# Performance work log

Hardware: AMD Instinct MI355X
Metric: run time of the kernel (lower is better)

## Reference

```python
import jax, jax.numpy as jnp
import numpy as np

NEG_INF = -9e15  # matches -9000000000000000.0 in the torch source


def setup_inputs() -> dict:
    key = jax.random.key(0)
    k1, k2, k3, k4 = jax.random.split(key, 4)
    B, H, N, D = 4, 8, 2048, 64
    queries = jax.random.normal(k1, (B, H, N, D), dtype=jnp.float32)
    keys = jax.random.normal(k2, (B, H, N, D), dtype=jnp.float32)
    values = jax.random.normal(k3, (B, H, N, D), dtype=jnp.float32)
    adj = jax.random.randint(k4, (N, N), 0, 2, dtype=jnp.int32)
    return {"queries": queries, "keys": keys, "values": values, "adj": adj}


def reference(queries, keys, values, adj):
    B, H, N, D = queries.shape
    # e = Q K^T / 8  (hard-coded divisor == sqrt(64))
    e = jnp.einsum("bhnd,bhmd->bhnm", queries, keys) / 8.0
    # graph-adjacency mask (adj [N,N] broadcasts over batch and heads)
    att = jnp.where(adj > 0, e, NEG_INF)
    att = jax.nn.softmax(att, axis=-1)
    # dropout p=0.0 / eval mode -> identity
    h_prime = jnp.einsum("bhnm,bhmd->bhnd", att, values)  # [B,H,N,D]
    # original uses .view (flat reshape), NOT a permute
    return h_prime.reshape(N, B, H, D)
```

## Files before the change

kernel.cpp:

```cpp
#include <hip/hip_runtime.h>
#include <math.h>

typedef short short8 __attribute__((ext_vector_type(8)));
typedef float float4_t __attribute__((ext_vector_type(4)));
typedef unsigned uint2_t __attribute__((ext_vector_type(2)));
typedef unsigned short ushort_t;

#define BH   32
#define N_   2048
#define D_   64
#define NCH  32
#define LDP  72
#define KV_ELEMS (BH * N_ * D_)
#define OFF_VF  (KV_ELEMS * 2)
#define OFF_MSK (KV_ELEMS * 4)
#define QSCALE 0.18033688f

__device__ __forceinline__ unsigned pack_bf16(float a, float b) {
  union { float f; unsigned u; } ua{a}, ub{b};
  return __builtin_amdgcn_perm(ub.u + 0x8000u, ua.u + 0x8000u, 0x07060302u);
}

__global__ __launch_bounds__(256) void prep_kernel(
    const float* __restrict__ K, const float* __restrict__ V,
    const int* __restrict__ adj, ushort_t* __restrict__ Kf,
    ushort_t* __restrict__ Vf, unsigned long long* __restrict__ msk) {
  __shared__ __align__(16) float Tc[64 * 68];
  const int blk = blockIdx.x, t = threadIdx.x;

  if (blk < 2048) {
    const bool isK = blk < 1024;
    const int b = isK ? blk : blk - 1024;
    const float* src = (isK ? K : V) + (b >> 5) * (N_ * D_) + (b & 31) * 64 * D_;
#pragma unroll
    for (int i = 0; i < 4; ++i) {
      int idx = i * 256 + t;
      int row = idx >> 4, c4 = (idx & 15) * 4;
      *(float4_t*)&Tc[row * 68 + c4] = *(const float4_t*)(src + row * D_ + c4);
    }
    __syncthreads();
    ushort_t* dst = (isK ? Kf : Vf) + b * 4096;
#pragma unroll
    for (int e = 0; e < 2; ++e) {
      int u = t * 2 + e;
      int g = u >> 6, lane = u & 63;
      int ks = g >> 2, quad = lane >> 4, l16 = lane & 15;
      float v[8];
      if (isK) {
        int nt = g & 3;
        const float* rp = &Tc[(nt * 16 + l16) * 68 + ks * 32 + quad * 8];
        float4_t a = *(const float4_t*)(rp);
        float4_t bq = *(const float4_t*)(rp + 4);
#pragma unroll
        for (int j = 0; j < 4; ++j) { v[j] = a[j]; v[4 + j] = bq[j]; }
      } else {
        int dt = g & 3, d = dt * 16 + l16;
#pragma unroll
        for (int j = 0; j < 8; ++j) {
          int key = 16 * (j & 3) + ks * 8 + quad * 2 + (j >> 2);
          v[j] = Tc[key * 68 + d];
        }
      }
      union { short8 s; unsigned u4[4]; } h;
      h.u4[0] = pack_bf16(v[0], v[1]); h.u4[1] = pack_bf16(v[2], v[3]);
      h.u4[2] = pack_bf16(v[4], v[5]); h.u4[3] = pack_bf16(v[6], v[7]);
      *(short8*)(dst + u * 8) = h.s;
    }
  } else {
    const int row = (blk - 2048) * 4 + (t >> 6);
    const int lane = t & 63;
    unsigned long long keep = 0;
#pragma unroll 8
    for (int i = 0; i < 32; ++i) {
      int a = adj[row * N_ + i * 64 + lane];
      unsigned long long b = __ballot(a > 0);
      if (lane == i) keep = b;
    }
    if (lane < 32) msk[row * 32 + lane] = keep;
  }
}

__global__ __launch_bounds__(128) void attn_main(
    const float* __restrict__ Q, const ushort_t* __restrict__ Kf,
    const ushort_t* __restrict__ Vf, const unsigned long long* __restrict__ msk,
    float* __restrict__ O) {
  __shared__ __align__(16) ushort_t kbuf[512 * 8];
  __shared__ __align__(16) ushort_t vbuf[512 * 8];
  __shared__ __align__(16) ushort_t lds_p[2][2][16 * LDP];

  const int t    = threadIdx.x;
  const int w    = t >> 6;
  const int lane = t & 63;
  const int quad = lane >> 4;
  const int l16  = lane & 15;
  const int bh   = blockIdx.x & (BH - 1);
  const int qt   = blockIdx.x >> 5;
  const int base = bh * (N_ * D_);
  const int qrow0 = qt * 64 + w * 32;

  const ushort_t* Kfb = Kf + (bh * 32) * 4096;
  const ushort_t* Vfb = Vf + (bh * 32) * 4096;

  short8 qf[2][2];
#pragma unroll
  for (int qg = 0; qg < 2; ++qg)
#pragma unroll
    for (int ks = 0; ks < 2; ++ks) {
      const float* qp = Q + base + (qrow0 + qg * 16 + l16) * D_ + ks * 32 + quad * 8;
      float4_t f0 = *(const float4_t*)(qp);
      float4_t f1 = *(const float4_t*)(qp + 4);
      union { short8 s; unsigned u[4]; } h;
      h.u[0] = pack_bf16(f0[0] * QSCALE, f0[1] * QSCALE);
      h.u[1] = pack_bf16(f0[2] * QSCALE, f0[3] * QSCALE);
      h.u[2] = pack_bf16(f1[0] * QSCALE, f1[1] * QSCALE);
      h.u[3] = pack_bf16(f1[2] * QSCALE, f1[3] * QSCALE);
      qf[qg][ks] = h.s;
    }

  float4_t oacc[2][4];
  float lsum[2][4];
#pragma unroll
  for (int qg = 0; qg < 2; ++qg) {
#pragma unroll
    for (int dt = 0; dt < 4; ++dt) oacc[qg][dt] = (float4_t){0.f, 0.f, 0.f, 0.f};
#pragma unroll
    for (int r = 0; r < 4; ++r) lsum[qg][r] = 0.f;
  }

  for (int c = 0; c < NCH; ++c) {
    __syncthreads();

    const ushort_t* kg = Kfb + c * 4096;
    const ushort_t* vg = Vfb + c * 4096;
#pragma unroll
    for (int i = 0; i < 4; ++i) {
      int u = i * 128 + t;
      *(short8*)(kbuf + u * 8) = *(const short8*)(kg + u * 8);
      *(short8*)(vbuf + u * 8) = *(const short8*)(vg + u * 8);
    }
    __syncthreads();

    short8 kf[4][2], vf[4][2];
#pragma unroll
    for (int nt = 0; nt < 4; ++nt)
#pragma unroll
      for (int ks = 0; ks < 2; ++ks) {
        kf[nt][ks] = *(const short8*)(kbuf + ((ks * 4 + nt) * 64 + lane) * 8);
        vf[nt][ks] = *(const short8*)(vbuf + ((ks * 4 + nt) * 64 + lane) * 8);
      }

    float4_t sacc[2][4];
#pragma unroll
    for (int qg = 0; qg < 2; ++qg)
#pragma unroll
      for (int nt = 0; nt < 4; ++nt) {
        float4_t acc = (float4_t){0.f, 0.f, 0.f, 0.f};
#pragma unroll
        for (int ks = 0; ks < 2; ++ks)
          acc = __builtin_amdgcn_mfma_f32_16x16x32_bf16(qf[qg][ks], kf[nt][ks], acc, 0, 0, 0);
        sacc[qg][nt] = acc;
      }

#pragma unroll
    for (int qg = 0; qg < 2; ++qg) {
      const int qrowq = qrow0 + qg * 16 + quad * 4;
#pragma unroll
      for (int r = 0; r < 4; ++r) {
        unsigned long long m = msk[(qrowq + r) * 32 + c];
        unsigned long long sh = m >> l16;
        unsigned lo = (unsigned)sh, hi = (unsigned)(sh >> 32);
        float p0 = (lo & 1u)       ? exp2f(sacc[qg][0][r]) : 0.f;
        float p1 = (lo & 0x10000u) ? exp2f(sacc[qg][1][r]) : 0.f;
        float p2 = (hi & 1u)       ? exp2f(sacc[qg][2][r]) : 0.f;
        float p3 = (hi & 0x10000u) ? exp2f(sacc[qg][3][r]) : 0.f;
        lsum[qg][r] += (p0 + p1) + (p2 + p3);
        uint2_t d2;
        d2.x = pack_bf16(p0, p1);
        d2.y = pack_bf16(p2, p3);
        *(uint2_t*)&lds_p[w][qg][(quad * 4 + r) * LDP + (l16 << 2)] = d2;
      }
    }

#pragma unroll
    for (int qg = 0; qg < 2; ++qg)
#pragma unroll
      for (int ks = 0; ks < 2; ++ks) {
        short8 pf = *(const short8*)&lds_p[w][qg][l16 * LDP + ks * 32 + quad * 8];
#pragma unroll
        for (int dt = 0; dt < 4; ++dt)
          oacc[qg][dt] = __builtin_amdgcn_mfma_f32_16x16x32_bf16(pf, vf[dt][ks], oacc[qg][dt], 0, 0, 0);
      }
  }

#pragma unroll
  for (int qg = 0; qg < 2; ++qg)
#pragma unroll
    for (int r = 0; r < 4; ++r) {
      float l = lsum[qg][r];
      l += __shfl_xor(l, 1);
      l += __shfl_xor(l, 2);
      l += __shfl_xor(l, 4);
      l += __shfl_xor(l, 8);
      float inv = 1.f / l;
      int qi = qrow0 + qg * 16 + quad * 4 + r;
#pragma unroll
      for (int dt = 0; dt < 4; ++dt)
        O[base + qi * D_ + dt * 16 + l16] = oacc[qg][dt][r] * inv;
    }
}

extern "C" void kernel_launch(void* const* d_in, const int* in_sizes, int n_in,
                              void* d_out, int out_size, void* d_ws, size_t ws_size,
                              hipStream_t stream) {
  const float* Q  = (const float*)d_in[0];
  const float* K  = (const float*)d_in[1];
  const float* V  = (const float*)d_in[2];
  const int* adj  = (const int*)d_in[3];
  float* O        = (float*)d_out;
  ushort_t* Kf    = (ushort_t*)d_ws;
  ushort_t* Vf    = (ushort_t*)((char*)d_ws + OFF_VF);
  unsigned long long* msk = (unsigned long long*)((char*)d_ws + OFF_MSK);

  prep_kernel<<<2560, 256, 0, stream>>>(K, V, adj, Kf, Vf, msk);
  attn_main<<<1024, 128, 0, stream>>>(Q, Kf, Vf, msk, O);
}
```

Before: 188.8 us.

## Load K/V fragments directly from global, drop LDS staging and block barriers

The attention kernel now uses 256 threads per block, with each wave handling 16 query rows instead of 32. K and V MFMA fragments are read straight from global memory in their pre-swizzled layout, so the shared-memory staging buffers and both __syncthreads per chunk are gone. The goal is to cut barrier stalls and LDS traffic and to raise occupancy through launch bounds (256,4) and fewer registers. The cost is that every wave now fetches the full K/V chunk from global/L2 on its own, which raises cache traffic and halves K/V reuse per wave.

```diff
diff --git a/kernel.cpp b/kernel.cpp
--- a/kernel.cpp
+++ b/kernel.cpp
@@ -80,13 +80,11 @@
   }
 }
 
-__global__ __launch_bounds__(128) void attn_main(
+__global__ __launch_bounds__(256, 4) void attn_main(
     const float* __restrict__ Q, const ushort_t* __restrict__ Kf,
     const ushort_t* __restrict__ Vf, const unsigned long long* __restrict__ msk,
     float* __restrict__ O) {
-  __shared__ __align__(16) ushort_t kbuf[512 * 8];
-  __shared__ __align__(16) ushort_t vbuf[512 * 8];
-  __shared__ __align__(16) ushort_t lds_p[2][2][16 * LDP];
+  __shared__ __align__(16) ushort_t lds_p[4][16 * LDP];
 
   const int t    = threadIdx.x;
   const int w    = t >> 6;
@@ -96,117 +94,98 @@
   const int bh   = blockIdx.x & (BH - 1);
   const int qt   = blockIdx.x >> 5;
   const int base = bh * (N_ * D_);
-  const int qrow0 = qt * 64 + w * 32;
+  const int qrow0 = qt * 64 + w * 16;
 
   const ushort_t* Kfb = Kf + (bh * 32) * 4096;
   const ushort_t* Vfb = Vf + (bh * 32) * 4096;
-
-  short8 qf[2][2];
-#pragma unroll
-  for (int qg = 0; qg < 2; ++qg)
-#pragma unroll
-    for (int ks = 0; ks < 2; ++ks) {
-      const float* qp = Q + base + (qrow0 + qg * 16 + l16) * D_ + ks * 32 + quad * 8;
-      float4_t f0 = *(const float4_t*)(qp);
-      float4_t f1 = *(const float4_t*)(qp + 4);
-      union { short8 s; unsigned u[4]; } h;
-      h.u[0] = pack_bf16(f0[0] * QSCALE, f0[1] * QSCALE);
-      h.u[1] = pack_bf16(f0[2] * QSCALE, f0[3] * QSCALE);
-      h.u[2] = pack_bf16(f1[0] * QSCALE, f1[1] * QSCALE);
-      h.u[3] = pack_bf16(f1[2] * QSCALE, f1[3] * QSCALE);
-      qf[qg][ks] = h.s;
-    }
-
-  float4_t oacc[2][4];
-  float lsum[2][4];
-#pragma unroll
-  for (int qg = 0; qg < 2; ++qg) {
-#pragma unroll
-    for (int dt = 0; dt < 4; ++dt) oacc[qg][dt] = (float4_t){0.f, 0.f, 0.f, 0.f};
-#pragma unroll
-    for (int r = 0; r < 4; ++r) lsum[qg][r] = 0.f;
-  }
+  const unsigned long long* mrow = msk + (qrow0 + quad * 4) * 32;
+
+  short8 qf[2];
+#pragma unroll
+  for (int ks = 0; ks < 2; ++ks) {
+    const float* qp = Q + base + (qrow0 + l16) * D_ + ks * 32 + quad * 8;
+    float4_t f0 = *(const float4_t*)(qp);
+    float4_t f1 = *(const float4_t*)(qp + 4);
+    union { short8 s; unsigned u[4]; } h;
+    h.u[0] = pack_bf16(f0[0] * QSCALE, f0[1] * QSCALE);
+    h.u[1] = pack_bf16(f0[2] * QSCALE, f0[3] * QSCALE);
+    h.u[2] = pack_bf16(f1[0] * QSCALE, f1[1] * QSCALE);
+    h.u[3] = pack_bf16(f1[2] * QSCALE, f1[3] * QSCALE);
+    qf[ks] = h.s;
+  }
+
+  float4_t oacc[4];
+  float lsum[4];
+#pragma unroll
+  for (int dt = 0; dt < 4; ++dt) oacc[dt] = (float4_t){0.f, 0.f, 0.f, 0.f};
+#pragma unroll
+  for (int r = 0; r < 4; ++r) lsum[r] = 0.f;
+
+  const int fo = lane * 8;
 
   for (int c = 0; c < NCH; ++c) {
-    __syncthreads();
-
     const ushort_t* kg = Kfb + c * 4096;
     const ushort_t* vg = Vfb + c * 4096;
-#pragma unroll
-    for (int i = 0; i < 4; ++i) {
-      int u = i * 128 + t;
-      *(short8*)(kbuf + u * 8) = *(const short8*)(kg + u * 8);
-      *(short8*)(vbuf + u * 8) = *(const short8*)(vg + u * 8);
-    }
-    __syncthreads();
-
-    short8 kf[4][2], vf[4][2];
-#pragma unroll
-    for (int nt = 0; nt < 4; ++nt)
-#pragma unroll
-      for (int ks = 0; ks < 2; ++ks) {
-        kf[nt][ks] = *(const short8*)(kbuf + ((ks * 4 + nt) * 64 + lane) * 8);
-        vf[nt][ks] = *(const short8*)(vbuf + ((ks * 4 + nt) * 64 + lane) * 8);
-      }
-
-    float4_t sacc[2][4];
-#pragma unroll
-    for (int qg = 0; qg < 2; ++qg)
-#pragma unroll
-      for (int nt = 0; nt < 4; ++nt) {
-        float4_t acc = (float4_t){0.f, 0.f, 0.f, 0.f};
-#pragma unroll
-        for (int ks = 0; ks < 2; ++ks)
-          acc = __builtin_amdgcn_mfma_f32_16x16x32_bf16(qf[qg][ks], kf[nt][ks], acc, 0, 0, 0);
-        sacc[qg][nt] = acc;
-      }
-
-#pragma unroll
-    for (int qg = 0; qg < 2; ++qg) {
-      const int qrowq = qrow0 + qg * 16 + quad * 4;
-#pragma unroll
-      for (int r = 0; r < 4; ++r) {
-        unsigned long long m = msk[(qrowq + r) * 32 + c];
-        unsigned long long sh = m >> l16;
-        unsigned lo = (unsigned)sh, hi = (unsigned)(sh >> 32);
-        float p0 = (lo & 1u)       ? exp2f(sacc[qg][0][r]) : 0.f;
-        float p1 = (lo & 0x10000u) ? exp2f(sacc[qg][1][r]) : 0.f;
-        float p2 = (hi & 1u)       ? exp2f(sacc[qg][2][r]) : 0.f;
-        float p3 = (hi & 0x10000u) ? exp2f(sacc[qg][3][r]) : 0.f;
-        lsum[qg][r] += (p0 + p1) + (p2 + p3);
-        uint2_t d2;
-        d2.x = pack_bf16(p0, p1);
-        d2.y = pack_bf16(p2, p3);
-        *(uint2_t*)&lds_p[w][qg][(quad * 4 + r) * LDP + (l16 << 2)] = d2;
-      }
-    }
-
-#pragma unroll
-    for (int qg = 0; qg < 2; ++qg)
-#pragma unroll
-      for (int ks = 0; ks < 2; ++ks) {
-        short8 pf = *(const short8*)&lds_p[w][qg][l16 * LDP + ks * 32 + quad * 8];
-#pragma unroll
-        for (int dt = 0; dt < 4; ++dt)
-          oacc[qg][dt] = __builtin_amdgcn_mfma_f32_16x16x32_bf16(pf, vf[dt][ks], oacc[qg][dt], 0, 0, 0);
-      }
-  }
-
-#pragma unroll
-  for (int qg = 0; qg < 2; ++qg)
+
+    unsigned long long mw[4];
+#pragma unroll
+    for (int r = 0; r < 4; ++r) mw[r] = mrow[r * 32 + c];
+
+    float4_t sacc[4];
+#pragma unroll
+    for (int nt = 0; nt < 4; ++nt) sacc[nt] = (float4_t){0.f, 0.f, 0.f, 0.f};
+#pragma unroll
+    for (int ks = 0; ks < 2; ++ks) {
+      short8 kfr[4];
+#pragma unroll
+      for (int nt = 0; nt < 4; ++nt)
+        kfr[nt] = *(const short8*)(kg + (ks * 4 + nt) * 512 + fo);
+#pragma unroll
+      for (int nt = 0; nt < 4; ++nt)
+        sacc[nt] = __builtin_amdgcn_mfma_f32_16x16x32_bf16(qf[ks], kfr[nt], sacc[nt], 0, 0, 0);
+    }
+
 #pragma unroll
     for (int r = 0; r < 4; ++r) {
-      float l = lsum[qg][r];
-      l += __shfl_xor(l, 1);
-      l += __shfl_xor(l, 2);
-      l += __shfl_xor(l, 4);
-      l += __shfl_xor(l, 8);
-      float inv = 1.f / l;
-      int qi = qrow0 + qg * 16 + quad * 4 + r;
+      unsigned long long sh = mw[r] >> l16;
+      unsigned lo = (unsigned)sh, hi = (unsigned)(sh >> 32);
+      float p0 = (lo & 1u)       ? exp2f(sacc[0][r]) : 0.f;
+      float p1 = (lo & 0x10000u) ? exp2f(sacc[1][r]) : 0.f;
+      float p2 = (hi & 1u)       ? exp2f(sacc[2][r]) : 0.f;
+      float p3 = (hi & 0x10000u) ? exp2f(sacc[3][r]) : 0.f;
+      lsum[r] += (p0 + p1) + (p2 + p3);
+      uint2_t d2;
+      d2.x = pack_bf16(p0, p1);
+      d2.y = pack_bf16(p2, p3);
+      *(uint2_t*)&lds_p[w][(quad * 4 + r) * LDP + (l16 << 2)] = d2;
+    }
+
+#pragma unroll
+    for (int ks = 0; ks < 2; ++ks) {
+      short8 vfr[4];
 #pragma unroll
       for (int dt = 0; dt < 4; ++dt)
-        O[base + qi * D_ + dt * 16 + l16] = oacc[qg][dt][r] * inv;
-    }
+        vfr[dt] = *(const short8*)(vg + (ks * 4 + dt) * 512 + fo);
+      short8 pf = *(const short8*)&lds_p[w][l16 * LDP + ks * 32 + quad * 8];
+#pragma unroll
+      for (int dt = 0; dt < 4; ++dt)
+        oacc[dt] = __builtin_amdgcn_mfma_f32_16x16x32_bf16(pf, vfr[dt], oacc[dt], 0, 0, 0);
+    }
+  }
+
+#pragma unroll
+  for (int r = 0; r < 4; ++r) {
+    float l = lsum[r];
+    l += __shfl_xor(l, 1);
+    l += __shfl_xor(l, 2);
+    l += __shfl_xor(l, 4);
+    l += __shfl_xor(l, 8);
+    float inv = 1.f / l;
+    int qi = qrow0 + quad * 4 + r;
+#pragma unroll
+    for (int dt = 0; dt < 4; ++dt)
+      O[base + qi * D_ + dt * 16 + l16] = oacc[dt][r] * inv;
+  }
 }
 
 extern "C" void kernel_launch(void* const* d_in, const int* in_sizes, int n_in,
@@ -222,5 +201,5 @@
   unsigned long long* msk = (unsigned long long*)((char*)d_ws + OFF_MSK);
 
   prep_kernel<<<2560, 256, 0, stream>>>(K, V, adj, Kf, Vf, msk);
-  attn_main<<<1024, 128, 0, stream>>>(Q, Kf, Vf, msk, O);
-}
+  attn_main<<<1024, 256, 0, stream>>>(Q, Kf, Vf, msk, O);
+}
```

Measured after the change: 188.7 us. About the same (-0.1%).

## Load K/V fragments directly from global, compute row sums via MFMA, use 4-wave blocks

Applied to the files above, without the earlier changes.

Drops the LDS staging of K/V chunks and the two block barriers per chunk; each wave now loads its pre-swizzled bf16 K/V fragments straight from global memory (relying on L2/L1 reuse across the four waves). The softmax denominator is computed by an extra MFMA against a ones vector instead of scalar accumulation plus cross-lane shuffles. Blocks grow to 256 threads covering 128 query rows, halving the grid, and mask words are prefetched per chunk. The risk is more global/L1 traffic per wave and higher register pressure from holding all fragments in registers.

```diff
diff --git a/kernel.cpp b/kernel.cpp
--- a/kernel.cpp
+++ b/kernel.cpp
@@ -80,13 +80,11 @@
   }
 }
 
-__global__ __launch_bounds__(128) void attn_main(
+__global__ __launch_bounds__(256, 2) void attn_main(
     const float* __restrict__ Q, const ushort_t* __restrict__ Kf,
     const ushort_t* __restrict__ Vf, const unsigned long long* __restrict__ msk,
     float* __restrict__ O) {
-  __shared__ __align__(16) ushort_t kbuf[512 * 8];
-  __shared__ __align__(16) ushort_t vbuf[512 * 8];
-  __shared__ __align__(16) ushort_t lds_p[2][2][16 * LDP];
+  __shared__ __align__(16) ushort_t lds_p[4][2][16 * LDP];
 
   const int t    = threadIdx.x;
   const int w    = t >> 6;
@@ -96,10 +94,14 @@
   const int bh   = blockIdx.x & (BH - 1);
   const int qt   = blockIdx.x >> 5;
   const int base = bh * (N_ * D_);
-  const int qrow0 = qt * 64 + w * 32;
+  const int qrow0 = qt * 128 + w * 32;
 
   const ushort_t* Kfb = Kf + (bh * 32) * 4096;
   const ushort_t* Vfb = Vf + (bh * 32) * 4096;
+  const unsigned long long* mr[2] = {
+    msk + (qrow0 + quad * 4) * 32,
+    msk + (qrow0 + 16 + quad * 4) * 32
+  };
 
   short8 qf[2][2];
 #pragma unroll
@@ -117,63 +119,58 @@
       qf[qg][ks] = h.s;
     }
 
+  short8 ones;
+#pragma unroll
+  for (int j = 0; j < 8; ++j) ones[j] = (short)0x3F80;
+
   float4_t oacc[2][4];
-  float lsum[2][4];
+  float4_t osum[2];
 #pragma unroll
   for (int qg = 0; qg < 2; ++qg) {
 #pragma unroll
     for (int dt = 0; dt < 4; ++dt) oacc[qg][dt] = (float4_t){0.f, 0.f, 0.f, 0.f};
-#pragma unroll
-    for (int r = 0; r < 4; ++r) lsum[qg][r] = 0.f;
+    osum[qg] = (float4_t){0.f, 0.f, 0.f, 0.f};
   }
 
+  const int fo = lane * 8;
+
   for (int c = 0; c < NCH; ++c) {
-    __syncthreads();
-
     const ushort_t* kg = Kfb + c * 4096;
     const ushort_t* vg = Vfb + c * 4096;
-#pragma unroll
-    for (int i = 0; i < 4; ++i) {
-      int u = i * 128 + t;
-      *(short8*)(kbuf + u * 8) = *(const short8*)(kg + u * 8);
-      *(short8*)(vbuf + u * 8) = *(const short8*)(vg + u * 8);
-    }
-    __syncthreads();
-
-    short8 kf[4][2], vf[4][2];
-#pragma unroll
-    for (int nt = 0; nt < 4; ++nt)
-#pragma unroll
-      for (int ks = 0; ks < 2; ++ks) {
-        kf[nt][ks] = *(const short8*)(kbuf + ((ks * 4 + nt) * 64 + lane) * 8);
-        vf[nt][ks] = *(const short8*)(vbuf + ((ks * 4 + nt) * 64 + lane) * 8);
-      }
-
-    float4_t sacc[2][4];
+
+    short8 kfr[2][4], vfr[2][4];
+#pragma unroll
+    for (int ks = 0; ks < 2; ++ks)
+#pragma unroll
+      for (int nt = 0; nt < 4; ++nt) {
+        kfr[ks][nt] = *(const short8*)(kg + (ks * 4 + nt) * 512 + fo);
+        vfr[ks][nt] = *(const short8*)(vg + (ks * 4 + nt) * 512 + fo);
+      }
+    unsigned long long mw[2][4];
 #pragma unroll
     for (int qg = 0; qg < 2; ++qg)
 #pragma unroll
-      for (int nt = 0; nt < 4; ++nt) {
-        float4_t acc = (float4_t){0.f, 0.f, 0.f, 0.f};
-#pragma unroll
-        for (int ks = 0; ks < 2; ++ks)
-          acc = __builtin_amdgcn_mfma_f32_16x16x32_bf16(qf[qg][ks], kf[nt][ks], acc, 0, 0, 0);
-        sacc[qg][nt] = acc;
-      }
+      for (int r = 0; r < 4; ++r) mw[qg][r] = mr[qg][r * 32 + c];
 
 #pragma unroll
     for (int qg = 0; qg < 2; ++qg) {
-      const int qrowq = qrow0 + qg * 16 + quad * 4;
+      float4_t sacc[4];
+#pragma unroll
+      for (int nt = 0; nt < 4; ++nt) sacc[nt] = (float4_t){0.f, 0.f, 0.f, 0.f};
+#pragma unroll
+      for (int ks = 0; ks < 2; ++ks)
+#pragma unroll
+        for (int nt = 0; nt < 4; ++nt)
+          sacc[nt] = __builtin_amdgcn_mfma_f32_16x16x32_bf16(qf[qg][ks], kfr[ks][nt], sacc[nt], 0, 0, 0);
+
 #pragma unroll
       for (int r = 0; r < 4; ++r) {
-        unsigned long long m = msk[(qrowq + r) * 32 + c];
-        unsigned long long sh = m >> l16;
+        unsigned long long sh = mw[qg][r] >> l16;
         unsigned lo = (unsigned)sh, hi = (unsigned)(sh >> 32);
-        float p0 = (lo & 1u)       ? exp2f(sacc[qg][0][r]) : 0.f;
-        float p1 = (lo & 0x10000u) ? exp2f(sacc[qg][1][r]) : 0.f;
-        float p2 = (hi & 1u)       ? exp2f(sacc[qg][2][r]) : 0.f;
-        float p3 = (hi & 0x10000u) ? exp2f(sacc[qg][3][r]) : 0.f;
-        lsum[qg][r] += (p0 + p1) + (p2 + p3);
+        float p0 = (lo & 1u)       ? exp2f(sacc[0][r]) : 0.f;
+        float p1 = (lo & 0x10000u) ? exp2f(sacc[1][r]) : 0.f;
+        float p2 = (hi & 1u)       ? exp2f(sacc[2][r]) : 0.f;
+        float p3 = (hi & 0x10000u) ? exp2f(sacc[3][r]) : 0.f;
         uint2_t d2;
         d2.x = pack_bf16(p0, p1);
         d2.y = pack_bf16(p2, p3);
@@ -188,7 +185,8 @@
         short8 pf = *(const short8*)&lds_p[w][qg][l16 * LDP + ks * 32 + quad * 8];
 #pragma unroll
         for (int dt = 0; dt < 4; ++dt)
-          oacc[qg][dt] = __builtin_amdgcn_mfma_f32_16x16x32_bf16(pf, vf[dt][ks], oacc[qg][dt], 0, 0, 0);
+          oacc[qg][dt] = __builtin_amdgcn_mfma_f32_16x16x32_bf16(pf, vfr[ks][dt], oacc[qg][dt], 0, 0, 0);
+        osum[qg] = __builtin_amdgcn_mfma_f32_16x16x32_bf16(pf, ones, osum[qg], 0, 0, 0);
       }
   }
 
@@ -196,12 +194,7 @@
   for (int qg = 0; qg < 2; ++qg)
 #pragma unroll
     for (int r = 0; r < 4; ++r) {
-      float l = lsum[qg][r];
-      l += __shfl_xor(l, 1);
-      l += __shfl_xor(l, 2);
-      l += __shfl_xor(l, 4);
-      l += __shfl_xor(l, 8);
-      float inv = 1.f / l;
+      float inv = 1.f / osum[qg][r];
       int qi = qrow0 + qg * 16 + quad * 4 + r;
 #pragma unroll
       for (int dt = 0; dt < 4; ++dt)
@@ -222,5 +215,5 @@
   unsigned long long* msk = (unsigned long long*)((char*)d_ws + OFF_MSK);
 
   prep_kernel<<<2560, 256, 0, stream>>>(K, V, adj, Kf, Vf, msk);
-  attn_main<<<1024, 128, 0, stream>>>(Q, Kf, Vf, msk, O);
-}
+  attn_main<<<512, 256, 0, stream>>>(Q, Kf, Vf, msk, O);
+}
```

Result: faster. 183.5 us (-2.8%).
